# Kernel tuning notes

Measured on AMD Instinct MI355X. Metric: run time of the kernel, lower is better.

The kernel has to match this reference:

```python
import jax, jax.numpy as jnp
import numpy as np

# Config (Mamba2-2.7B-like)
HID = 2048          # hidden_size
EXPAND = 2
INTER = EXPAND * HID   # 4096
NH = 64             # num_heads
HD = 64             # head_dim (NH*HD == INTER)
NG = 8              # n_groups
SS = 128            # state_size
CK = 4              # conv_kernel
CH = 256            # chunk_size
EPS = 1e-6
CONV_DIM = INTER + 2 * NG * SS          # 6144
PROJ = INTER + CONV_DIM + NH            # 10304
B_SZ, SEQ = 2, 2048


def segment_sum(x):
    # x: [..., T] -> [..., T, T]; stable cumulative-sum based segment sums
    T = x.shape[-1]
    x = jnp.repeat(x[..., None], T, axis=-1)
    x = jnp.where(jnp.tril(jnp.ones((T, T), dtype=bool), k=-1), x, 0.0)
    s = jnp.cumsum(x, axis=-2)
    return jnp.where(jnp.tril(jnp.ones((T, T), dtype=bool), k=0), s, -jnp.inf)


def setup_inputs() -> dict:
    key = jax.random.key(0)
    ks = jax.random.split(key, 6)
    sc = 0.02
    return {
        "input_states": jax.random.normal(ks[0], (B_SZ, SEQ, HID), dtype=jnp.float32),
        "in_proj_w": jax.random.normal(ks[1], (HID, PROJ), dtype=jnp.float32) * sc,
        "conv_w": jax.random.normal(ks[2], (CK, 1, CONV_DIM), dtype=jnp.float32) * sc,  # WIO, depthwise
        "conv_b": jnp.zeros((CONV_DIM,), dtype=jnp.float32),
        "dt_bias": jnp.ones((NH,), dtype=jnp.float32),
        "A_log": jnp.log(jnp.arange(1, NH + 1, dtype=jnp.float32)),
        "D": jnp.ones((NH,), dtype=jnp.float32),
        "norm_w": jnp.ones((INTER,), dtype=jnp.float32),
        "out_proj_w": jax.random.normal(ks[3], (INTER, HID), dtype=jnp.float32) * sc,
    }


def reference(input_states, in_proj_w, conv_w, conv_b, dt_bias, A_log, D, norm_w, out_proj_w):
    b, s, _ = input_states.shape
    proj = input_states @ in_proj_w                                   # [b,s,PROJ]
    gate, hBC, dt = jnp.split(proj, [INTER, INTER + CONV_DIM], axis=-1)

    # depthwise causal-ish conv (flax nn.Conv with padding='SAME', groups=CONV_DIM)
    hBC = jax.lax.conv_general_dilated(
        hBC, conv_w, window_strides=(1,), padding="SAME",
        dimension_numbers=("NWC", "WIO", "NWC"), feature_group_count=CONV_DIM,
    ) + conv_b
    hBC = jax.nn.silu(hBC)[:, :s]
    hs, Bmat, Cmat = jnp.split(hBC, [INTER, INTER + NG * SS], axis=-1)

    A = -jnp.exp(A_log.astype(jnp.float32))                           # [h]
    dt = jax.nn.softplus(dt + dt_bias)                                # [b,s,h]
    dt = jnp.maximum(dt, 0.0)                                         # time_step_limit (0, inf)

    hs = hs.reshape(b, s, NH, HD).astype(jnp.float32)                 # [b,s,h,p]
    Bmat = Bmat.reshape(b, s, NG, SS).astype(jnp.float32)
    Cmat = Cmat.reshape(b, s, NG, SS).astype(jnp.float32)
    Bmat = jnp.repeat(Bmat, NH // NG, axis=2)                         # [b,s,h,n]
    Cmat = jnp.repeat(Cmat, NH // NG, axis=2)

    pad = (CH - s % CH) % CH

    def to_chunks(t):
        t = jnp.pad(t, [(0, 0), (0, pad)] + [(0, 0)] * (t.ndim - 2))
        return t.reshape(b, -1, CH, *t.shape[2:])

    D_res = D[None, None, :, None] * jnp.pad(hs, [(0, 0), (0, pad), (0, 0), (0, 0)])

    hs_dt = hs * dt[..., None]                                        # discretize x
    A_bt = A[None, None, :] * dt                                      # [b,s,h]

    hs_c = to_chunks(hs_dt)                                           # [b,c,l,h,p]
    A_c = to_chunks(A_bt)                                             # [b,c,l,h]
    B_c = to_chunks(Bmat)                                             # [b,c,l,h,n]
    C_c = to_chunks(Cmat)

    A_p = jnp.transpose(A_c, (0, 3, 1, 2))                            # [b,h,c,l]
    A_cum = jnp.cumsum(A_p, axis=-1)

    # 1. intra-chunk (diagonal blocks)
    L = jnp.exp(segment_sum(A_p))                                     # [b,h,c,l,l]
    M = jnp.einsum("bclhn,bcshn->bclsh", C_c, B_c) * jnp.transpose(L, (0, 2, 3, 4, 1))
    Y_diag = jnp.einsum("bclsh,bcshp->bclhp", M, hs_c)

    # 2. intra-chunk states
    decay_states = jnp.exp(A_cum[..., -1:] - A_cum)                   # [b,h,c,l]
    B_decay = B_c * jnp.transpose(decay_states, (0, 2, 3, 1))[..., None]
    states = jnp.einsum("bclhn,bclhp->bchpn", B_decay, hs_c)          # [b,c,h,p,n]

    # 3. inter-chunk recurrence
    states = jnp.concatenate([jnp.zeros_like(states[:, :1]), states], axis=1)  # [b,c+1,h,p,n]
    A_last = jnp.pad(A_cum[..., -1], [(0, 0), (0, 0), (1, 0)])        # [b,h,c+1]
    decay_chunk = jnp.exp(segment_sum(A_last))                        # [b,h,c+1,c+1]
    new_states = jnp.einsum("bhij,bjhpn->bihpn", decay_chunk, states)
    states_out = new_states[:, :-1]                                   # [b,c,h,p,n]

    # 4. state -> output
    state_decay_out = jnp.exp(A_cum)                                  # [b,h,c,l]
    Y_off = jnp.einsum("bclhn,bchpn->bclhp", C_c, states_out) \
        * jnp.transpose(state_decay_out, (0, 2, 3, 1))[..., None]

    y = (Y_diag + Y_off).reshape(b, -1, NH, HD) + D_res
    y = y[:, :s].reshape(b, s, INTER)

    # gated RMSNorm
    yf = y.astype(jnp.float32) * jax.nn.silu(gate.astype(jnp.float32))
    var = jnp.mean(jnp.square(yf), axis=-1, keepdims=True)
    yn = norm_w * (yf * jax.lax.rsqrt(var + EPS))

    return (yn.astype(input_states.dtype)) @ out_proj_w
```

## Files before the change

kernel.cpp:

```cpp
#include <hip/hip_runtime.h>
#include <hip/hip_bf16.h>


#define S_LEN 2048
#define HIDDEN 2048
#define INTER 4096
#define NH 64
#define HD 64
#define NG 8
#define SSZ 128
#define CONV_DIM 6144
#define PROJ_DIM 10304
#define PROJ_PAD 10496
#define NC 8
#define CHK 256
#define ROWS 4096
#define DT_OFF 10240
#define B_OFF 4096
#define C_OFF 5120

typedef __hip_bfloat16 bf16;
typedef __attribute__((ext_vector_type(8))) short bf16x8;
typedef __attribute__((ext_vector_type(4))) float f32x4;
#define MFMA16(a, b, c) __builtin_amdgcn_mfma_f32_16x16x32_bf16(a, b, c, 0, 0, 0)

union U16x8 { uint4 u; bf16x8 v; };

__device__ __forceinline__ float siluf(float x) { return x / (1.f + __expf(-x)); }
__device__ __forceinline__ float ldf(const float* p) { return *p; }
__device__ __forceinline__ float ldf(const bf16* p) { return __bfloat162float(*p); }
__device__ __forceinline__ unsigned short f2bu(float x) {
  bf16 h = __float2bfloat16(x);
  return __builtin_bit_cast(unsigned short, h);
}
__device__ __forceinline__ float bu2f(unsigned short u) {
  return __uint_as_float(((unsigned)u) << 16);
}
__device__ __forceinline__ unsigned pack2(float lo, float hi) {
  return ((unsigned)f2bu(hi) << 16) | f2bu(lo);
}
__device__ __forceinline__ void gload16(const void* g, void* l) {
  __builtin_amdgcn_global_load_lds((const __attribute__((address_space(1))) unsigned*)g,
                                   (__attribute__((address_space(3))) unsigned*)l, 16, 0, 0);
}

__global__ __launch_bounds__(256) void cvt_bf16_k(const float* __restrict__ x,
                                                  unsigned short* __restrict__ o, int n4) {
  int idx = blockIdx.x * 256 + threadIdx.x;
  int stride = gridDim.x * 256;
  for (int i = idx; i < n4; i += stride) {
    float4 v = reinterpret_cast<const float4*>(x)[i];
    uint2 u = make_uint2(pack2(v.x, v.y), pack2(v.z, v.w));
    reinterpret_cast<uint2*>(o)[i] = u;
  }
}

__global__ __launch_bounds__(256) void wT_k(const float* __restrict__ W,
                                            unsigned short* __restrict__ Wt,
                                            int K, int N) {
  __shared__ unsigned short t[64][72];
  int n0 = blockIdx.x * 64, k0 = blockIdx.y * 64;
  int tid = threadIdx.x;
#pragma unroll
  for (int i = 0; i < 16; ++i) {
    int idx = tid + i * 256;
    int kr = idx >> 6, nc = idx & 63;
    float v = (n0 + nc < N) ? W[(size_t)(k0 + kr) * N + n0 + nc] : 0.f;
    t[kr][nc] = f2bu(v);
  }
  __syncthreads();
#pragma unroll
  for (int i = 0; i < 16; ++i) {
    int idx = tid + i * 256;
    int nr = idx >> 6, kc = idx & 63;
    Wt[(size_t)(n0 + nr) * K + k0 + kc] = t[kc][nr];
  }
}

__device__ __forceinline__ int mod9(int x) { return x >= 9 ? x - 9 : x; }

__device__ __forceinline__ void stage_half(const unsigned short* __restrict__ A,
                                           const unsigned short* __restrict__ Bt,
                                           unsigned short* lds9, int hj, int slot,
                                           int m0, int n0, int K, int hmax,
                                           int tid, int wid) {
  if (hj >= hmax) return;
  const int t = hj >> 2, i = hj & 3;
  const unsigned short* src = (i < 2) ? A : Bt;
  const int br = ((i < 2) ? m0 : n0) + (i & 1) * 128;
  const int g = (tid & 7) ^ ((tid >> 3) & 7);
#pragma unroll
  for (int r = 0; r < 2; ++r) {
    int row = r * 64 + (tid >> 3);
    gload16(&src[(size_t)(br + row) * K + t * 64 + g * 8],
            &lds9[slot * 8192 + r * 4096 + wid * 512]);
  }
}

template <typename TC>
__global__ __launch_bounds__(512, 2) void gemm_8ph(const unsigned short* __restrict__ A,
                                                   const unsigned short* __restrict__ Bt,
                                                   TC* __restrict__ C,
                                                   int M, int N, int K) {
  extern __shared__ unsigned short lds9[];
  const int tid = threadIdx.x;
  const int lane = tid & 63, hi = lane >> 4, sl = lane & 15;
  const int wid = tid >> 6;
  const int wm = wid >> 2, wn = wid & 3;
  const int gx = gridDim.x;
  int lin = blockIdx.y * gx + blockIdx.x;
  int cpx = (gx * gridDim.y) >> 3;
  int swz = (lin & 7) * cpx + (lin >> 3);
  const int m0 = (swz / gx) * 256;
  const int n0 = (swz % gx) * 256;
  const int NT = K >> 6;
  const int HMAX = NT << 2;
  const int rbB = (wn & 1) * 64;

  f32x4 acc[8][4] = {};
  bf16x8 a0[4][2], a1[4][2], bb[4][2];

#pragma unroll
  for (int j = 0; j < 5; ++j)
    stage_half(A, Bt, lds9, j, j, m0, n0, K, HMAX, tid, wid);

  int j0 = 0;
  for (int t = 0; t < NT; ++t) {
    const int sAw = mod9(j0 + wm);
    const int sBw = mod9(j0 + 2 + (wn >> 1));
    asm volatile("s_waitcnt vmcnt(2)" ::: "memory");
    __builtin_amdgcn_sched_barrier(0);
    __builtin_amdgcn_s_barrier();
    __builtin_amdgcn_sched_barrier(0);
#pragma unroll
    for (int mf = 0; mf < 4; ++mf)
#pragma unroll
      for (int kk = 0; kk < 2; ++kk) {
        int ra = mf * 16 + sl;
        a0[mf][kk] = *reinterpret_cast<const bf16x8*>(
            &lds9[sAw * 8192 + ra * 64 + (((kk * 4 + hi) ^ (ra & 7)) * 8)]);
      }
#pragma unroll
    for (int nf = 0; nf < 2; ++nf)
#pragma unroll
      for (int kk = 0; kk < 2; ++kk) {
        int rb = rbB + nf * 16 + sl;
        bb[nf][kk] = *reinterpret_cast<const bf16x8*>(
            &lds9[sBw * 8192 + rb * 64 + (((kk * 4 + hi) ^ (rb & 7)) * 8)]);
      }
    stage_half(A, Bt, lds9, 4 * t + 5, mod9(j0 + 5), m0, n0, K, HMAX, tid, wid);
    asm volatile("s_waitcnt lgkmcnt(0)" ::: "memory");
    __builtin_amdgcn_sched_barrier(0);
    __builtin_amdgcn_s_setprio(1);
#pragma unroll
    for (int mf = 0; mf < 4; ++mf)
#pragma unroll
      for (int nf = 0; nf < 2; ++nf)
#pragma unroll
        for (int kk = 0; kk < 2; ++kk)
          acc[mf][nf] = MFMA16(a0[mf][kk], bb[nf][kk], acc[mf][nf]);
    __builtin_amdgcn_s_setprio(0);
    __builtin_amdgcn_sched_barrier(0);
#pragma unroll
    for (int nf = 2; nf < 4; ++nf)
#pragma unroll
      for (int kk = 0; kk < 2; ++kk) {
        int rb = rbB + nf * 16 + sl;
        bb[nf][kk] = *reinterpret_cast<const bf16x8*>(
            &lds9[sBw * 8192 + rb * 64 + (((kk * 4 + hi) ^ (rb & 7)) * 8)]);
      }
    stage_half(A, Bt, lds9, 4 * t + 6, mod9(j0 + 6), m0, n0, K, HMAX, tid, wid);
    asm volatile("s_waitcnt lgkmcnt(0)" ::: "memory");
    __builtin_amdgcn_sched_barrier(0);
    __builtin_amdgcn_s_setprio(1);
#pragma unroll
    for (int mf = 0; mf < 4; ++mf)
#pragma unroll
      for (int nf = 2; nf < 4; ++nf)
#pragma unroll
        for (int kk = 0; kk < 2; ++kk)
          acc[mf][nf] = MFMA16(a0[mf][kk], bb[nf][kk], acc[mf][nf]);
    __builtin_amdgcn_s_setprio(0);
    __builtin_amdgcn_sched_barrier(0);
#pragma unroll
    for (int mf = 0; mf < 4; ++mf)
#pragma unroll
      for (int kk = 0; kk < 2; ++kk) {
        int ra = (mf + 4) * 16 + sl;
        a1[mf][kk] = *reinterpret_cast<const bf16x8*>(
            &lds9[sAw * 8192 + ra * 64 + (((kk * 4 + hi) ^ (ra & 7)) * 8)]);
      }
    stage_half(A, Bt, lds9, 4 * t + 7, mod9(j0 + 7), m0, n0, K, HMAX, tid, wid);
    asm volatile("s_waitcnt lgkmcnt(0)" ::: "memory");
    __builtin_amdgcn_sched_barrier(0);
    __builtin_amdgcn_s_setprio(1);
#pragma unroll
    for (int mf = 0; mf < 4; ++mf)
#pragma unroll
      for (int nf = 0; nf < 2; ++nf)
#pragma unroll
        for (int kk = 0; kk < 2; ++kk)
          acc[mf + 4][nf] = MFMA16(a1[mf][kk], bb[nf][kk], acc[mf + 4][nf]);
    __builtin_amdgcn_s_setprio(0);
    __builtin_amdgcn_sched_barrier(0);
    stage_half(A, Bt, lds9, 4 * t + 8, mod9(j0 + 8), m0, n0, K, HMAX, tid, wid);
    __builtin_amdgcn_s_setprio(1);
#pragma unroll
    for (int mf = 0; mf < 4; ++mf)
#pragma unroll
      for (int nf = 2; nf < 4; ++nf)
#pragma unroll
        for (int kk = 0; kk < 2; ++kk)
          acc[mf + 4][nf] = MFMA16(a1[mf][kk], bb[nf][kk], acc[mf + 4][nf]);
    __builtin_amdgcn_s_setprio(0);
    __builtin_amdgcn_sched_barrier(0);
    j0 += 4; if (j0 >= 9) j0 -= 9;
  }
#pragma unroll
  for (int mf = 0; mf < 8; ++mf)
#pragma unroll
    for (int nf = 0; nf < 4; ++nf) {
      int col = n0 + wn * 64 + nf * 16 + sl;
      if (col < N) {
#pragma unroll
        for (int r = 0; r < 4; ++r) {
          int row = m0 + wm * 128 + mf * 16 + hi * 4 + r;
          if constexpr (sizeof(TC) == 2)
            C[(size_t)row * N + col] = __float2bfloat16(acc[mf][nf][r]);
          else
            C[(size_t)row * N + col] = acc[mf][nf][r];
        }
      }
    }
}

template <int BN, typename TC>
__global__ __launch_bounds__(256) void gemm_bf16(const unsigned short* __restrict__ A,
                                                 const unsigned short* __restrict__ Bt,
                                                 TC* __restrict__ C,
                                                 int M, int N, int K) {
  __shared__ __align__(16) unsigned short sA[128 * 64];
  __shared__ __align__(16) unsigned short sB[BN * 64];
  const int tid = threadIdx.x;
  const int lane = tid & 63, hi = lane >> 4, sl = lane & 15;
  const int wid = tid >> 6, wm = wid >> 1, wn = wid & 1;
  const int gx = gridDim.x;
  int lin = blockIdx.y * gx + blockIdx.x;
  int cpx = (gx * gridDim.y) >> 3;
  int swz = (lin & 7) * cpx + (lin >> 3);
  const int m0 = (swz / gx) * 128;
  const int n0 = (swz % gx) * BN;
  const int lrow = lane >> 3;
  const int lslot = lane & 7;
  constexpr int NCH = 16 + BN / 8;
  constexpr int PER = NCH / 4;
  constexpr int FN = BN / 32;

  f32x4 acc[4][FN] = {};
  for (int kt = 0; kt < K; kt += 64) {
    __syncthreads();
#pragma unroll
    for (int i = 0; i < PER; ++i) {
      int ch = wid * PER + i;
      if (ch < 16) {
        int r = ch * 8 + lrow;
        int g = lslot ^ (r & 7);
        gload16(&A[(size_t)(m0 + r) * K + kt + g * 8], &sA[ch * 512]);
      } else {
        int r = (ch - 16) * 8 + lrow;
        int g = lslot ^ (r & 7);
        gload16(&Bt[(size_t)(n0 + r) * K + kt + g * 8], &sB[(ch - 16) * 512]);
      }
    }
    __syncthreads();
#pragma unroll
    for (int su = 0; su < 2; ++su) {
      bf16x8 af[4], bfr[FN];
#pragma unroll
      for (int m = 0; m < 4; ++m) {
        int r = wm * 64 + m * 16 + sl;
        af[m] = *reinterpret_cast<const bf16x8*>(
            &sA[r * 64 + (((su * 4 + hi) ^ (r & 7)) * 8)]);
      }
#pragma unroll
      for (int j = 0; j < FN; ++j) {
        int r = wn * (BN / 2) + j * 16 + sl;
        bfr[j] = *reinterpret_cast<const bf16x8*>(
            &sB[r * 64 + (((su * 4 + hi) ^ (r & 7)) * 8)]);
      }
#pragma unroll
      for (int m = 0; m < 4; ++m)
#pragma unroll
        for (int j = 0; j < FN; ++j)
          acc[m][j] = MFMA16(af[m], bfr[j], acc[m][j]);
    }
  }
#pragma unroll
  for (int m = 0; m < 4; ++m)
#pragma unroll
    for (int j = 0; j < FN; ++j) {
      int col = n0 + wn * (BN / 2) + j * 16 + sl;
      if (col < N) {
#pragma unroll
        for (int r = 0; r < 4; ++r) {
          int row = m0 + wm * 64 + m * 16 + hi * 4 + r;
          if constexpr (sizeof(TC) == 2)
            C[(size_t)row * N + col] = __float2bfloat16(acc[m][j][r]);
          else
            C[(size_t)row * N + col] = acc[m][j][r];
        }
      }
    }
}

__global__ __launch_bounds__(256) void conv_silu_k(const bf16* __restrict__ proj,
                                                   const float* __restrict__ cw,
                                                   const float* __restrict__ cb,
                                                   bf16* __restrict__ convo) {
  int idx = blockIdx.x * 256 + threadIdx.x;
  int ci = idx % (CONV_DIM / 8);
  int row = idx / (CONV_DIM / 8);
  int c8 = ci * 8;
  int t = row & (S_LEN - 1);
  int b = row >> 11;
  float acc[8];
  {
    float4 b0 = *reinterpret_cast<const float4*>(&cb[c8]);
    float4 b1 = *reinterpret_cast<const float4*>(&cb[c8 + 4]);
    acc[0] = b0.x; acc[1] = b0.y; acc[2] = b0.z; acc[3] = b0.w;
    acc[4] = b1.x; acc[5] = b1.y; acc[6] = b1.z; acc[7] = b1.w;
  }
#pragma unroll
  for (int w = 0; w < 4; w++) {
    int tt = t + w - 1;
    if (tt >= 0 && tt < S_LEN) {
      U16x8 u;
      u.u = *reinterpret_cast<const uint4*>(
          &proj[(size_t)(b * S_LEN + tt) * PROJ_DIM + INTER + c8]);
      float4 w0 = *reinterpret_cast<const float4*>(&cw[w * CONV_DIM + c8]);
      float4 w1 = *reinterpret_cast<const float4*>(&cw[w * CONV_DIM + c8 + 4]);
      acc[0] += w0.x * bu2f((unsigned short)u.v[0]);
      acc[1] += w0.y * bu2f((unsigned short)u.v[1]);
      acc[2] += w0.z * bu2f((unsigned short)u.v[2]);
      acc[3] += w0.w * bu2f((unsigned short)u.v[3]);
      acc[4] += w1.x * bu2f((unsigned short)u.v[4]);
      acc[5] += w1.y * bu2f((unsigned short)u.v[5]);
      acc[6] += w1.z * bu2f((unsigned short)u.v[6]);
      acc[7] += w1.w * bu2f((unsigned short)u.v[7]);
    }
  }
  uint4 o;
  o.x = pack2(siluf(acc[0]), siluf(acc[1]));
  o.y = pack2(siluf(acc[2]), siluf(acc[3]));
  o.z = pack2(siluf(acc[4]), siluf(acc[5]));
  o.w = pack2(siluf(acc[6]), siluf(acc[7]));
  *reinterpret_cast<uint4*>(&convo[(size_t)row * CONV_DIM + c8]) = o;
}

__global__ __launch_bounds__(256) void dt_k(const bf16* __restrict__ proj,
                                            const float* __restrict__ dtb,
                                            float* __restrict__ dtp) {
  int idx = blockIdx.x * 256 + threadIdx.x;
  int h = idx & 63;
  int row = idx >> 6;
  float x = ldf(&proj[(size_t)row * PROJ_DIM + DT_OFF + h]) + dtb[h];
  dtp[idx] = (x > 20.f) ? x : log1pf(__expf(x));
}

__global__ __launch_bounds__(256) void acum_k(const float* __restrict__ dtp,
                                              const float* __restrict__ alog,
                                              float* __restrict__ acum) {
  __shared__ float buf[2][CHK];
  int blk = blockIdx.x;
  int c = blk & 7;
  int h = (blk >> 3) & 63;
  int b = blk >> 9;
  int tid = threadIdx.x;
  int row0 = b * S_LEN + c * CHK;
  float a = -__expf(alog[h]);
  buf[0][tid] = a * dtp[(size_t)(row0 + tid) * NH + h];
  __syncthreads();
  int cur = 0;
#pragma unroll
  for (int off = 1; off < 256; off <<= 1) {
    float nv = buf[cur][tid];
    if (tid >= off) nv += buf[cur][tid - off];
    buf[cur ^ 1][tid] = nv;
    cur ^= 1;
    __syncthreads();
  }
  acum[(size_t)blk * CHK + tid] = buf[cur][tid];
}

__global__ __launch_bounds__(256) void chunk_states_mfma(const bf16* __restrict__ convo,
                                                         const float* __restrict__ dtp,
                                                         const float* __restrict__ acum,
                                                         float* __restrict__ cs) {
  __shared__ float sAc[CHK];
  __shared__ float sDtf[CHK];
  __shared__ float sEx[64];
  __shared__ __align__(16) unsigned short sHT[64 * 64];
  __shared__ __align__(16) unsigned short sBd[128 * 64];
  const int tid = threadIdx.x;
  const int lane = tid & 63, hi = lane >> 4, sl = lane & 15;
  const int wid = tid >> 6, wm = wid >> 1, wn = wid & 1;
  const int blk = blockIdx.x;
  const int h = blk & 63, bc = blk >> 6, c = bc & 7, b = bc >> 3, g = h >> 3;
  const int row0 = b * S_LEN + c * CHK;
  sAc[tid] = acum[((size_t)((b * NH + h) * NC + c)) * CHK + tid];
  sDtf[tid] = dtp[(size_t)(row0 + tid) * NH + h];
  f32x4 acc[2][4] = {};
  for (int ts = 0; ts < 4; ++ts) {
    __syncthreads();
    if (tid < 64) sEx[tid] = __expf(sAc[CHK - 1] - sAc[ts * 64 + tid]);
    __syncthreads();
#pragma unroll
    for (int it = 0; it < 2; ++it) {
      int cid = tid + it * 256;
      int t = cid >> 3, p8 = (cid & 7) * 8;
      U16x8 u;
      u.u = *reinterpret_cast<const uint4*>(
          &convo[(size_t)(row0 + ts * 64 + t) * CONV_DIM + h * HD + p8]);
      float dtv = sDtf[ts * 64 + t];
#pragma unroll
      for (int e = 0; e < 8; ++e) {
        int p = p8 + e;
        int G = (p & 7) ^ ((p >> 3) & 7);
        sHT[p * 64 + (((t >> 3) ^ G) * 8) + (t & 7)] =
            f2bu(bu2f((unsigned short)u.v[e]) * dtv);
      }
    }
#pragma unroll
    for (int it = 0; it < 4; ++it) {
      int cid = tid + it * 256;
      int t = cid >> 4, n8 = (cid & 15) * 8;
      U16x8 u;
      u.u = *reinterpret_cast<const uint4*>(
          &convo[(size_t)(row0 + ts * 64 + t) * CONV_DIM + B_OFF + g * SSZ + n8]);
      float ex = sEx[t];
#pragma unroll
      for (int e = 0; e < 8; ++e) {
        int n = n8 + e;
        int G = (n & 7) ^ ((n >> 3) & 7);
        sBd[n * 64 + (((t >> 3) ^ G) * 8) + (t & 7)] =
            f2bu(bu2f((unsigned short)u.v[e]) * ex);
      }
    }
    __syncthreads();
#pragma unroll
    for (int kc = 0; kc < 2; ++kc) {
      bf16x8 a[2], bb[4];
#pragma unroll
      for (int m = 0; m < 2; ++m) {
        int p = wm * 32 + m * 16 + sl;
        int G = (p & 7) ^ ((p >> 3) & 7);
        a[m] = *reinterpret_cast<const bf16x8*>(
            &sHT[p * 64 + (((kc * 4 + hi) ^ G) * 8)]);
      }
#pragma unroll
      for (int j = 0; j < 4; ++j) {
        int n = wn * 64 + j * 16 + sl;
        int G = (n & 7) ^ ((n >> 3) & 7);
        bb[j] = *reinterpret_cast<const bf16x8*>(
            &sBd[n * 64 + (((kc * 4 + hi) ^ G) * 8)]);
      }
#pragma unroll
      for (int m = 0; m < 2; ++m)
#pragma unroll
        for (int j = 0; j < 4; ++j) acc[m][j] = MFMA16(a[m], bb[j], acc[m][j]);
    }
  }
  size_t base = (size_t)blk * HD * SSZ;
#pragma unroll
  for (int m = 0; m < 2; ++m)
#pragma unroll
    for (int j = 0; j < 4; ++j)
#pragma unroll
      for (int r = 0; r < 4; ++r) {
        int p = wm * 32 + m * 16 + hi * 4 + r;
        int n = wn * 64 + j * 16 + sl;
        cs[base + (size_t)p * SSZ + n] = acc[m][j][r];
      }
}

__global__ __launch_bounds__(256) void chunk_rec_k(const float* __restrict__ acum,
                                                   float* __restrict__ cs) {
  int idx = blockIdx.x * 256 + threadIdx.x;
  int n = idx & 127;
  int p = (idx >> 7) & 63;
  int h = (idx >> 13) & 63;
  int b = idx >> 19;
  float run = 0.f;
#pragma unroll
  for (int c = 0; c < NC; c++) {
    size_t off = ((size_t)(((b * NC + c) * NH + h) * HD + p)) * SSZ + n;
    float csv = cs[off];
    float al = acum[((size_t)((b * NH + h) * NC + c)) * CHK + (CHK - 1)];
    cs[off] = run;
    run = run * __expf(al) + csv;
  }
}

__global__ __launch_bounds__(256) void chunk_out_mfma(const bf16* __restrict__ convo,
                                                      const float* __restrict__ dtp,
                                                      const float* __restrict__ acum,
                                                      const float* __restrict__ cs,
                                                      const float* __restrict__ Dp,
                                                      bf16* __restrict__ yb) {
  __shared__ float sAc[CHK];
  __shared__ float sDt[CHK];
  __shared__ __align__(16) unsigned short sB[64 * 128];
  __shared__ __align__(16) unsigned short sH[64 * 64];
  __shared__ __align__(16) unsigned short sW[4 * 64 * 64];
  const int tid = threadIdx.x;
  const int lane = tid & 63, hi = lane >> 4, sl = lane & 15;
  const int wid = tid >> 6;
  const int blk = blockIdx.x;
  const int h = blk & 63;
  const int bc = blk >> 6;
  const int c = bc & 7;
  const int b = bc >> 3;
  const int g = h >> 3;
  const int row0 = b * S_LEN + c * CHK;
  unsigned short* sWp = &sW[wid * 4096];

  sAc[tid] = acum[((size_t)((b * NH + h) * NC + c)) * CHK + tid];
  sDt[tid] = dtp[(size_t)(row0 + tid) * NH + h];

  bf16x8 cf[4][4];
#pragma unroll
  for (int m = 0; m < 4; ++m)
#pragma unroll
    for (int kc = 0; kc < 4; ++kc) {
      int l = wid * 64 + m * 16 + sl;
      U16x8 u;
      u.u = *reinterpret_cast<const uint4*>(
          &convo[(size_t)(row0 + l) * CONV_DIM + C_OFF + g * SSZ + kc * 32 + hi * 8]);
      cf[m][kc] = u.v;
    }

  f32x4 acc[4][4] = {};

  for (int st = 0; st < 4; ++st) {
    __syncthreads();
#pragma unroll
    for (int it = 0; it < 4; ++it) {
      int cid = tid + it * 256;
      int s = cid >> 4, gr = cid & 15;
      const uint4* p = reinterpret_cast<const uint4*>(
          &convo[(size_t)(row0 + st * 64 + s) * CONV_DIM + B_OFF + g * SSZ + gr * 8]);
      *reinterpret_cast<uint4*>(&sB[s * 128 + (gr ^ (s & 7)) * 8]) = *p;
    }
#pragma unroll
    for (int it = 0; it < 16; ++it) {
      int cid = tid + it * 256;
      int s = cid >> 6, pp = cid & 63;
      float v = ldf(&convo[(size_t)(row0 + st * 64 + s) * CONV_DIM + h * HD + pp]) *
                sDt[st * 64 + s];
      sH[pp * 64 + (((s >> 3) ^ (pp & 7)) * 8) + (s & 7)] = f2bu(v);
    }
    __syncthreads();
    if (wid >= st) {
#pragma unroll
      for (int sf = 0; sf < 4; ++sf) {
        f32x4 d[4] = {};
#pragma unroll
        for (int kc = 0; kc < 4; ++kc) {
          int srow = sf * 16 + sl;
          bf16x8 bfv = *reinterpret_cast<const bf16x8*>(
              &sB[srow * 128 + (((kc * 4 + hi) ^ (srow & 7)) * 8)]);
#pragma unroll
          for (int m = 0; m < 4; ++m) d[m] = MFMA16(cf[m][kc], bfv, d[m]);
        }
        int s_loc = sf * 16 + sl;
        int s_glob = st * 64 + s_loc;
        float acS = sAc[s_glob];
        bool diag = (st == wid);
#pragma unroll
        for (int m = 0; m < 4; ++m)
#pragma unroll
          for (int r = 0; r < 4; ++r) {
            int l_loc = m * 16 + hi * 4 + r;
            int l_glob = wid * 64 + l_loc;
            float e = __expf(sAc[l_glob] - acS);
            float v = d[m][r] * e;
            if (diag && s_glob > l_glob) v = 0.f;
            sWp[l_loc * 64 + (((s_loc >> 3) ^ (l_loc & 7)) * 8) + (s_loc & 7)] = f2bu(v);
          }
      }
    }
    __syncthreads();
    if (wid >= st) {
#pragma unroll
      for (int kc = 0; kc < 2; ++kc) {
        bf16x8 a[4], bb[4];
#pragma unroll
        for (int m = 0; m < 4; ++m) {
          int l = m * 16 + sl;
          a[m] = *reinterpret_cast<const bf16x8*>(
              &sWp[l * 64 + (((kc * 4 + hi) ^ (l & 7)) * 8)]);
        }
#pragma unroll
        for (int j = 0; j < 4; ++j) {
          int p = j * 16 + sl;
          bb[j] = *reinterpret_cast<const bf16x8*>(
              &sH[p * 64 + (((kc * 4 + hi) ^ (p & 7)) * 8)]);
        }
#pragma unroll
        for (int m = 0; m < 4; ++m)
#pragma unroll
          for (int j = 0; j < 4; ++j) acc[m][j] = MFMA16(a[m], bb[j], acc[m][j]);
      }
    }
  }

  __syncthreads();
  {
    size_t sinbase = ((size_t)(((b * NC + c) * NH + h) * HD)) * SSZ;
#pragma unroll
    for (int it = 0; it < 8; ++it) {
      int cid = tid + it * 256;
      int p = cid >> 5, q = cid & 31;
      float4 v = *reinterpret_cast<const float4*>(&cs[sinbase + (size_t)p * SSZ + q * 4]);
      uint2 val = make_uint2(pack2(v.x, v.y), pack2(v.z, v.w));
      *reinterpret_cast<uint2*>(&sB[p * 128 + ((q >> 1) ^ (p & 7)) * 8 + (q & 1) * 4]) = val;
    }
  }
  __syncthreads();
#pragma unroll
  for (int m = 0; m < 4; ++m) {
    float e = __expf(sAc[wid * 64 + m * 16 + sl]);
#pragma unroll
    for (int kc = 0; kc < 4; ++kc) {
      bf16x8 fv = cf[m][kc];
#pragma unroll
      for (int ei = 0; ei < 8; ++ei) {
        unsigned short us = (unsigned short)fv[ei];
        fv[ei] = (short)f2bu(bu2f(us) * e);
      }
      cf[m][kc] = fv;
    }
  }
#pragma unroll
  for (int kc = 0; kc < 4; ++kc) {
    bf16x8 bb[4];
#pragma unroll
    for (int j = 0; j < 4; ++j) {
      int p = j * 16 + sl;
      bb[j] = *reinterpret_cast<const bf16x8*>(
          &sB[p * 128 + (((kc * 4 + hi) ^ (p & 7)) * 8)]);
    }
#pragma unroll
    for (int m = 0; m < 4; ++m)
#pragma unroll
      for (int j = 0; j < 4; ++j) acc[m][j] = MFMA16(cf[m][kc], bb[j], acc[m][j]);
  }

  float Dh = Dp[h];
#pragma unroll
  for (int m = 0; m < 4; ++m)
#pragma unroll
    for (int j = 0; j < 4; ++j)
#pragma unroll
      for (int r = 0; r < 4; ++r) {
        int l_glob = wid * 64 + m * 16 + hi * 4 + r;
        size_t row = (size_t)(row0 + l_glob);
        int pg = j * 16 + sl;
        float hraw = ldf(&convo[row * CONV_DIM + h * HD + pg]);
        yb[row * INTER + h * HD + pg] = __float2bfloat16(acc[m][j][r] + Dh * hraw);
      }
}

__global__ __launch_bounds__(256) void norm_k(const bf16* __restrict__ proj,
                                              const float* __restrict__ nw,
                                              bf16* __restrict__ yb) {
  int row = blockIdx.x;
  int tid = threadIdx.x;
  float vals[16];
  float ss = 0.f;
#pragma unroll
  for (int half = 0; half < 2; half++) {
    int colb = tid * 8 + half * 2048;
    U16x8 gy, gg;
    gy.u = *reinterpret_cast<const uint4*>(&yb[(size_t)row * INTER + colb]);
    gg.u = *reinterpret_cast<const uint4*>(&proj[(size_t)row * PROJ_DIM + colb]);
#pragma unroll
    for (int e = 0; e < 8; e++) {
      float yf = bu2f((unsigned short)gy.v[e]) * siluf(bu2f((unsigned short)gg.v[e]));
      vals[half * 8 + e] = yf;
      ss += yf * yf;
    }
  }
#pragma unroll
  for (int off = 32; off > 0; off >>= 1) ss += __shfl_down(ss, off);
  __shared__ float red[4];
  if ((tid & 63) == 0) red[tid >> 6] = ss;
  __syncthreads();
  float tot = red[0] + red[1] + red[2] + red[3];
  float scale = rsqrtf(tot * (1.f / INTER) + 1e-6f);
#pragma unroll
  for (int half = 0; half < 2; half++) {
    int colb = tid * 8 + half * 2048;
    float4 w0 = *reinterpret_cast<const float4*>(&nw[colb]);
    float4 w1 = *reinterpret_cast<const float4*>(&nw[colb + 4]);
    float s0 = vals[half * 8 + 0] * scale * w0.x, s1 = vals[half * 8 + 1] * scale * w0.y;
    float s2 = vals[half * 8 + 2] * scale * w0.z, s3 = vals[half * 8 + 3] * scale * w0.w;
    float s4 = vals[half * 8 + 4] * scale * w1.x, s5 = vals[half * 8 + 5] * scale * w1.y;
    float s6 = vals[half * 8 + 6] * scale * w1.z, s7 = vals[half * 8 + 7] * scale * w1.w;
    uint4 o = make_uint4(pack2(s0, s1), pack2(s2, s3), pack2(s4, s5), pack2(s6, s7));
    *reinterpret_cast<uint4*>(&yb[(size_t)row * INTER + colb]) = o;
  }
}

extern "C" void kernel_launch(void* const* d_in, const int* in_sizes, int n_in,
                              void* d_out, int out_size, void* d_ws, size_t ws_size,
                              hipStream_t stream) {
  const float* x     = (const float*)d_in[0];
  const float* wproj = (const float*)d_in[1];
  const float* cw    = (const float*)d_in[2];
  const float* cb    = (const float*)d_in[3];
  const float* dtb   = (const float*)d_in[4];
  const float* alog  = (const float*)d_in[5];
  const float* Dp    = (const float*)d_in[6];
  const float* nw    = (const float*)d_in[7];
  const float* wout  = (const float*)d_in[8];
  float* out = (float*)d_out;
  char* ws = (char*)d_ws;

  bf16*  proj  = (bf16*)(ws);
  bf16*  convo = (bf16*)(ws + 84410368);
  bf16*  yb    = (bf16*)(ws + 134742016);
  float* dtp   = (float*)(ws + 168296448);
  float* acum  = (float*)(ws + 169345024);
  float* cs    = (float*)(ws + 170393600);
  unsigned short* Wt1 = (unsigned short*)(ws + 84410368);
  unsigned short* xb  = (unsigned short*)(ws + 134742016);
  unsigned short* Wt2 = (unsigned short*)(ws + 170393600);

  hipFuncSetAttribute(reinterpret_cast<const void*>(&gemm_8ph<bf16>),
                      hipFuncAttributeMaxDynamicSharedMemorySize, 147456);

  cvt_bf16_k<<<dim3(2048), 256, 0, stream>>>(x, xb, ROWS * HIDDEN / 4);
  wT_k<<<dim3(PROJ_PAD / 64, HIDDEN / 64), 256, 0, stream>>>(wproj, Wt1, HIDDEN, PROJ_DIM);
  gemm_8ph<bf16><<<dim3(PROJ_PAD / 256, ROWS / 256), 512, 147456, stream>>>(
      xb, Wt1, proj, ROWS, PROJ_DIM, HIDDEN);
  conv_silu_k<<<dim3(ROWS * CONV_DIM / 8 / 256), 256, 0, stream>>>(proj, cw, cb, convo);
  dt_k<<<dim3(ROWS * NH / 256), 256, 0, stream>>>(proj, dtb, dtp);
  acum_k<<<dim3(2 * NH * NC), 256, 0, stream>>>(dtp, alog, acum);
  chunk_states_mfma<<<dim3(2 * NC * NH), 256, 0, stream>>>(convo, dtp, acum, cs);
  chunk_rec_k<<<dim3(2 * NH * HD * SSZ / 256), 256, 0, stream>>>(acum, cs);
  chunk_out_mfma<<<dim3(2 * NC * NH), 256, 0, stream>>>(convo, dtp, acum, cs, Dp, yb);
  norm_k<<<dim3(ROWS), 256, 0, stream>>>(proj, nw, yb);
  wT_k<<<dim3(HIDDEN / 64, INTER / 64), 256, 0, stream>>>(wout, Wt2, INTER, HIDDEN);
  gemm_bf16<64, float><<<dim3(HIDDEN / 64, ROWS / 128), 256, 0, stream>>>(
      (const unsigned short*)yb, Wt2, out, ROWS, HIDDEN, INTER);
}
```

Before: 515.0 us.

## Use 8-phase GEMM with split-K for out_proj and sum partials

```diff
diff --git a/kernel.cpp b/kernel.cpp
--- a/kernel.cpp
+++ b/kernel.cpp
@@ -55,6 +55,19 @@
   }
 }
 
+__global__ __launch_bounds__(256) void add_k(const float* __restrict__ p0,
+                                             const float* __restrict__ p1,
+                                             float* __restrict__ o, int n4) {
+  int idx = blockIdx.x * 256 + threadIdx.x;
+  int stride = gridDim.x * 256;
+  for (int i = idx; i < n4; i += stride) {
+    float4 a = reinterpret_cast<const float4*>(p0)[i];
+    float4 b = reinterpret_cast<const float4*>(p1)[i];
+    reinterpret_cast<float4*>(o)[i] =
+        make_float4(a.x + b.x, a.y + b.y, a.z + b.z, a.w + b.w);
+  }
+}
+
 __global__ __launch_bounds__(256) void wT_k(const float* __restrict__ W,
                                             unsigned short* __restrict__ Wt,
                                             int K, int N) {
@@ -82,7 +95,7 @@
 __device__ __forceinline__ void stage_half(const unsigned short* __restrict__ A,
                                            const unsigned short* __restrict__ Bt,
                                            unsigned short* lds9, int hj, int slot,
-                                           int m0, int n0, int K, int hmax,
+                                           int m0, int n0, int K, int kbase, int hmax,
                                            int tid, int wid) {
   if (hj >= hmax) return;
   const int t = hj >> 2, i = hj & 3;
@@ -92,7 +105,7 @@
 #pragma unroll
   for (int r = 0; r < 2; ++r) {
     int row = r * 64 + (tid >> 3);
-    gload16(&src[(size_t)(br + row) * K + t * 64 + g * 8],
+    gload16(&src[(size_t)(br + row) * K + kbase + t * 64 + g * 8],
             &lds9[slot * 8192 + r * 4096 + wid * 512]);
   }
 }
@@ -101,7 +114,7 @@
 __global__ __launch_bounds__(512, 2) void gemm_8ph(const unsigned short* __restrict__ A,
                                                    const unsigned short* __restrict__ Bt,
                                                    TC* __restrict__ C,
-                                                   int M, int N, int K) {
+                                                   int M, int N, int K, int ksplit) {
   extern __shared__ unsigned short lds9[];
   const int tid = threadIdx.x;
   const int lane = tid & 63, hi = lane >> 4, sl = lane & 15;
@@ -113,7 +126,9 @@
   int swz = (lin & 7) * cpx + (lin >> 3);
   const int m0 = (swz / gx) * 256;
   const int n0 = (swz % gx) * 256;
-  const int NT = K >> 6;
+  const int kbase = blockIdx.z * ksplit;
+  TC* Cz = C + (size_t)blockIdx.z * M * N;
+  const int NT = ksplit >> 6;
   const int HMAX = NT << 2;
   const int rbB = (wn & 1) * 64;
 
@@ -122,7 +137,7 @@
 
 #pragma unroll
   for (int j = 0; j < 5; ++j)
-    stage_half(A, Bt, lds9, j, j, m0, n0, K, HMAX, tid, wid);
+    stage_half(A, Bt, lds9, j, j, m0, n0, K, kbase, HMAX, tid, wid);
 
   int j0 = 0;
   for (int t = 0; t < NT; ++t) {
@@ -148,7 +163,7 @@
         bb[nf][kk] = *reinterpret_cast<const bf16x8*>(
             &lds9[sBw * 8192 + rb * 64 + (((kk * 4 + hi) ^ (rb & 7)) * 8)]);
       }
-    stage_half(A, Bt, lds9, 4 * t + 5, mod9(j0 + 5), m0, n0, K, HMAX, tid, wid);
+    stage_half(A, Bt, lds9, 4 * t + 5, mod9(j0 + 5), m0, n0, K, kbase, HMAX, tid, wid);
     asm volatile("s_waitcnt lgkmcnt(0)" ::: "memory");
     __builtin_amdgcn_sched_barrier(0);
     __builtin_amdgcn_s_setprio(1);
@@ -169,7 +184,7 @@
         bb[nf][kk] = *reinterpret_cast<const bf16x8*>(
             &lds9[sBw * 8192 + rb * 64 + (((kk * 4 + hi) ^ (rb & 7)) * 8)]);
       }
-    stage_half(A, Bt, lds9, 4 * t + 6, mod9(j0 + 6), m0, n0, K, HMAX, tid, wid);
+    stage_half(A, Bt, lds9, 4 * t + 6, mod9(j0 + 6), m0, n0, K, kbase, HMAX, tid, wid);
     asm volatile("s_waitcnt lgkmcnt(0)" ::: "memory");
     __builtin_amdgcn_sched_barrier(0);
     __builtin_amdgcn_s_setprio(1);
@@ -190,7 +205,7 @@
         a1[mf][kk] = *reinterpret_cast<const bf16x8*>(
             &lds9[sAw * 8192 + ra * 64 + (((kk * 4 + hi) ^ (ra & 7)) * 8)]);
       }
-    stage_half(A, Bt, lds9, 4 * t + 7, mod9(j0 + 7), m0, n0, K, HMAX, tid, wid);
+    stage_half(A, Bt, lds9, 4 * t + 7, mod9(j0 + 7), m0, n0, K, kbase, HMAX, tid, wid);
     asm volatile("s_waitcnt lgkmcnt(0)" ::: "memory");
     __builtin_amdgcn_sched_barrier(0);
     __builtin_amdgcn_s_setprio(1);
@@ -203,7 +218,7 @@
           acc[mf + 4][nf] = MFMA16(a1[mf][kk], bb[nf][kk], acc[mf + 4][nf]);
     __builtin_amdgcn_s_setprio(0);
     __builtin_amdgcn_sched_barrier(0);
-    stage_half(A, Bt, lds9, 4 * t + 8, mod9(j0 + 8), m0, n0, K, HMAX, tid, wid);
+    stage_half(A, Bt, lds9, 4 * t + 8, mod9(j0 + 8), m0, n0, K, kbase, HMAX, tid, wid);
     __builtin_amdgcn_s_setprio(1);
 #pragma unroll
     for (int mf = 0; mf < 4; ++mf)
@@ -226,88 +241,9 @@
         for (int r = 0; r < 4; ++r) {
           int row = m0 + wm * 128 + mf * 16 + hi * 4 + r;
           if constexpr (sizeof(TC) == 2)
-            C[(size_t)row * N + col] = __float2bfloat16(acc[mf][nf][r]);
+            Cz[(size_t)row * N + col] = __float2bfloat16(acc[mf][nf][r]);
           else
-            C[(size_t)row * N + col] = acc[mf][nf][r];
-        }
-      }
-    }
-}
-
-template <int BN, typename TC>
-__global__ __launch_bounds__(256) void gemm_bf16(const unsigned short* __restrict__ A,
-                                                 const unsigned short* __restrict__ Bt,
-                                                 TC* __restrict__ C,
-                                                 int M, int N, int K) {
-  __shared__ __align__(16) unsigned short sA[128 * 64];
-  __shared__ __align__(16) unsigned short sB[BN * 64];
-  const int tid = threadIdx.x;
-  const int lane = tid & 63, hi = lane >> 4, sl = lane & 15;
-  const int wid = tid >> 6, wm = wid >> 1, wn = wid & 1;
-  const int gx = gridDim.x;
-  int lin = blockIdx.y * gx + blockIdx.x;
-  int cpx = (gx * gridDim.y) >> 3;
-  int swz = (lin & 7) * cpx + (lin >> 3);
-  const int m0 = (swz / gx) * 128;
-  const int n0 = (swz % gx) * BN;
-  const int lrow = lane >> 3;
-  const int lslot = lane & 7;
-  constexpr int NCH = 16 + BN / 8;
-  constexpr int PER = NCH / 4;
-  constexpr int FN = BN / 32;
-
-  f32x4 acc[4][FN] = {};
-  for (int kt = 0; kt < K; kt += 64) {
-    __syncthreads();
-#pragma unroll
-    for (int i = 0; i < PER; ++i) {
-      int ch = wid * PER + i;
-      if (ch < 16) {
-        int r = ch * 8 + lrow;
-        int g = lslot ^ (r & 7);
-        gload16(&A[(size_t)(m0 + r) * K + kt + g * 8], &sA[ch * 512]);
-      } else {
-        int r = (ch - 16) * 8 + lrow;
-        int g = lslot ^ (r & 7);
-        gload16(&Bt[(size_t)(n0 + r) * K + kt + g * 8], &sB[(ch - 16) * 512]);
-      }
-    }
-    __syncthreads();
-#pragma unroll
-    for (int su = 0; su < 2; ++su) {
-      bf16x8 af[4], bfr[FN];
-#pragma unroll
-      for (int m = 0; m < 4; ++m) {
-        int r = wm * 64 + m * 16 + sl;
-        af[m] = *reinterpret_cast<const bf16x8*>(
-            &sA[r * 64 + (((su * 4 + hi) ^ (r & 7)) * 8)]);
-      }
-#pragma unroll
-      for (int j = 0; j < FN; ++j) {
-        int r = wn * (BN / 2) + j * 16 + sl;
-        bfr[j] = *reinterpret_cast<const bf16x8*>(
-            &sB[r * 64 + (((su * 4 + hi) ^ (r & 7)) * 8)]);
-      }
-#pragma unroll
-      for (int m = 0; m < 4; ++m)
-#pragma unroll
-        for (int j = 0; j < FN; ++j)
-          acc[m][j] = MFMA16(af[m], bfr[j], acc[m][j]);
-    }
-  }
-#pragma unroll
-  for (int m = 0; m < 4; ++m)
-#pragma unroll
-    for (int j = 0; j < FN; ++j) {
-      int col = n0 + wn * (BN / 2) + j * 16 + sl;
-      if (col < N) {
-#pragma unroll
-        for (int r = 0; r < 4; ++r) {
-          int row = m0 + wm * 64 + m * 16 + hi * 4 + r;
-          if constexpr (sizeof(TC) == 2)
-            C[(size_t)row * N + col] = __float2bfloat16(acc[m][j][r]);
-          else
-            C[(size_t)row * N + col] = acc[m][j][r];
+            Cz[(size_t)row * N + col] = acc[mf][nf][r];
         }
       }
     }
@@ -736,14 +672,17 @@
   unsigned short* Wt1 = (unsigned short*)(ws + 84410368);
   unsigned short* xb  = (unsigned short*)(ws + 134742016);
   unsigned short* Wt2 = (unsigned short*)(ws + 170393600);
+  float* part = (float*)(ws);
 
   hipFuncSetAttribute(reinterpret_cast<const void*>(&gemm_8ph<bf16>),
                       hipFuncAttributeMaxDynamicSharedMemorySize, 147456);
+  hipFuncSetAttribute(reinterpret_cast<const void*>(&gemm_8ph<float>),
+                      hipFuncAttributeMaxDynamicSharedMemorySize, 147456);
 
   cvt_bf16_k<<<dim3(2048), 256, 0, stream>>>(x, xb, ROWS * HIDDEN / 4);
   wT_k<<<dim3(PROJ_PAD / 64, HIDDEN / 64), 256, 0, stream>>>(wproj, Wt1, HIDDEN, PROJ_DIM);
-  gemm_8ph<bf16><<<dim3(PROJ_PAD / 256, ROWS / 256), 512, 147456, stream>>>(
-      xb, Wt1, proj, ROWS, PROJ_DIM, HIDDEN);
+  gemm_8ph<bf16><<<dim3(PROJ_PAD / 256, ROWS / 256, 1), 512, 147456, stream>>>(
+      xb, Wt1, proj, ROWS, PROJ_DIM, HIDDEN, HIDDEN);
   conv_silu_k<<<dim3(ROWS * CONV_DIM / 8 / 256), 256, 0, stream>>>(proj, cw, cb, convo);
   dt_k<<<dim3(ROWS * NH / 256), 256, 0, stream>>>(proj, dtb, dtp);
   acum_k<<<dim3(2 * NH * NC), 256, 0, stream>>>(dtp, alog, acum);
@@ -752,6 +691,8 @@
   chunk_out_mfma<<<dim3(2 * NC * NH), 256, 0, stream>>>(convo, dtp, acum, cs, Dp, yb);
   norm_k<<<dim3(ROWS), 256, 0, stream>>>(proj, nw, yb);
   wT_k<<<dim3(HIDDEN / 64, INTER / 64), 256, 0, stream>>>(wout, Wt2, INTER, HIDDEN);
-  gemm_bf16<64, float><<<dim3(HIDDEN / 64, ROWS / 128), 256, 0, stream>>>(
-      (const unsigned short*)yb, Wt2, out, ROWS, HIDDEN, INTER);
-}
+  gemm_8ph<float><<<dim3(HIDDEN / 256, ROWS / 256, 2), 512, 147456, stream>>>(
+      (const unsigned short*)yb, Wt2, part, ROWS, HIDDEN, INTER, INTER / 2);
+  add_k<<<dim3(2048), 256, 0, stream>>>(part, part + (size_t)ROWS * HIDDEN, out,
+                                        ROWS * HIDDEN / 4);
+}
```

After: 503.7 us. -2.2%, faster.
